# Kernel tuning notes

Hardware: AMD Instinct MI355X
Metric: run time of the kernel (lower is better)

The kernel has to match this reference:

```python
import jax, jax.numpy as jnp
import numpy as np

B, S, IN_DIM, OUT_DIM = 4, 4096, 512, 64


def setup_inputs() -> dict:
    key = jax.random.key(0)
    ks = jax.random.split(key, 8)
    scale = 1.0 / np.sqrt(IN_DIM)
    return {
        "input_embedding": jax.random.normal(ks[0], (B, S, IN_DIM), dtype=jnp.float32),
        "mask": jax.random.randint(ks[1], (S, S), 0, 2, dtype=jnp.int32),
        "Wq": jax.random.uniform(ks[2], (IN_DIM, OUT_DIM), jnp.float32, -scale, scale),
        "bq": jax.random.uniform(ks[3], (OUT_DIM,), jnp.float32, -scale, scale),
        "Wk": jax.random.uniform(ks[4], (IN_DIM, OUT_DIM), jnp.float32, -scale, scale),
        "bk": jax.random.uniform(ks[5], (OUT_DIM,), jnp.float32, -scale, scale),
        "Wv": jax.random.uniform(ks[6], (IN_DIM, OUT_DIM), jnp.float32, -scale, scale),
        "bv": jax.random.uniform(ks[7], (OUT_DIM,), jnp.float32, -scale, scale),
    }


def reference(input_embedding, mask, Wq, bq, Wk, bk, Wv, bv):
    # q,k,v: [B,S,D]
    q = jnp.einsum("bsi,id->bsd", input_embedding, Wq) + bq
    k = jnp.einsum("bsi,id->bsd", input_embedding, Wk) + bk
    v = jnp.einsum("bsi,id->bsd", input_embedding, Wv) + bv
    d_k = q.shape[-1]
    # scores: [B,S,S]
    scores = jnp.einsum("bqd,bkd->bqk", q, k) / jnp.sqrt(jnp.float32(d_k))
    # NOTE: original uses masked_fill(mask==0, 1e-6) on the SCORES (not -inf)
    scores = jnp.where(mask == 0, jnp.float32(1e-6), scores)
    probs = jax.nn.softmax(scores, axis=-1)
    return jnp.einsum("bqk,bkd->bqd", probs, v)
```

## Files before the change

### kernel.cpp

```cpp
#include <hip/hip_runtime.h>

#define BATCH 4
#define SEQ 4096
#define IND 512
#define DH 64
#define NSPLIT 8
#define QKVB 1024
#define MASKB 1366

typedef __attribute__((ext_vector_type(8))) _Float16 f16x8;
typedef __attribute__((ext_vector_type(4))) _Float16 f16x4;
typedef __attribute__((ext_vector_type(4))) float f32x4;
typedef unsigned long long u64;
typedef unsigned int u32;

#define MFMA16(a, b, c) __builtin_amdgcn_mfma_f32_16x16x32_f16(a, b, c, 0, 0, 0)
#define GLL16(g, l)                                                                  \
    __builtin_amdgcn_global_load_lds(                                                \
        (const __attribute__((address_space(1))) void*)(g),                          \
        (__attribute__((address_space(3))) void*)(l), 16, 0, 0)

__global__ __launch_bounds__(256) void wprep_kernel(
    const float* __restrict__ Wq, const float* __restrict__ bq,
    const float* __restrict__ Wk, const float* __restrict__ bk,
    const float* __restrict__ Wv, const float* __restrict__ bv,
    _Float16* __restrict__ Wt, float* __restrict__ bcat) {
    __shared__ float tile[64][65];
    const int bid = blockIdx.x, tid = threadIdx.x;
    const int mat = bid >> 3, k0 = (bid & 7) * 64;
    const float QS = 0.125f * 1.44269504088896f;
    const float* W = (mat == 0) ? Wq : ((mat == 1) ? Wk : Wv);
    const float scale = (mat == 0) ? QS : 1.0f;
    if (bid == 0 && tid < 192) {
        int m2 = tid >> 6, n = tid & 63;
        const float* bb = (m2 == 0) ? bq : ((m2 == 1) ? bk : bv);
        bcat[tid] = bb[n] * ((m2 == 0) ? QS : 1.0f);
    }
    const int n = tid & 63, r0 = tid >> 6;
#pragma unroll
    for (int i = 0; i < 16; ++i) {
        int r = r0 * 16 + i;
        tile[r][n] = W[(size_t)(k0 + r) * 64 + n];
    }
    __syncthreads();
    const int k = tid & 63, n0 = tid >> 6;
#pragma unroll
    for (int i = 0; i < 16; ++i) {
        int nn = n0 * 16 + i;
        Wt[(size_t)(mat * 64 + nn) * IND + k0 + k] = (_Float16)(tile[k][nn] * scale);
    }
}

__global__ __launch_bounds__(192) void qkv_mask_kernel(const float* __restrict__ X,
    const _Float16* __restrict__ Wt, const float* __restrict__ bcat,
    _Float16* __restrict__ Qh, _Float16* __restrict__ Kh, _Float16* __restrict__ Vt,
    const int* __restrict__ mask, u64* __restrict__ bits3) {
    __shared__ __align__(16) _Float16 xs[16 * 520];
    const int tid = threadIdx.x;
    const int w = tid >> 6, lane = tid & 63, l15 = lane & 15, g = lane >> 4;

    if (blockIdx.x >= QKVB) {
        int wv = (blockIdx.x - QKVB) * 3 + w;
        if (wv < 4096) {
            int kw = wv & 63, q0 = (wv >> 6) * 64;
            u64 keep = 0;
#pragma unroll 8
            for (int i = 0; i < 64; ++i) {
                int val = mask[(size_t)(q0 + i) * SEQ + kw * 64 + lane];
                u64 b = __ballot(val != 0);
                if (lane == i) keep = b;
            }
            bits3[((size_t)kw << 12) + q0 + lane] = keep;
        }
        return;
    }

    const int m0 = blockIdx.x * 16;
    const float4* src = (const float4*)(X + (size_t)m0 * IND);
#pragma unroll
    for (int u = 0; u < 11; ++u) {
        int idx = u * 192 + tid;
        if (idx < 2048) {
            float4 x = src[idx];
            int row = idx >> 7, c4 = idx & 127;
            f16x4 h;
            h[0] = (_Float16)x.x; h[1] = (_Float16)x.y;
            h[2] = (_Float16)x.z; h[3] = (_Float16)x.w;
            *(f16x4*)&xs[row * 520 + c4 * 4] = h;
        }
    }
    __syncthreads();

    f32x4 acc[4];
#pragma unroll
    for (int nt = 0; nt < 4; ++nt) acc[nt] = (f32x4){0.f, 0.f, 0.f, 0.f};

    const _Float16* Wm = Wt + (size_t)(w * 64 + l15) * IND + g * 8;
#pragma unroll
    for (int kc = 0; kc < 16; ++kc) {
        f16x8 a = *(const f16x8*)&xs[l15 * 520 + kc * 32 + g * 8];
#pragma unroll
        for (int nt = 0; nt < 4; ++nt)
            acc[nt] = MFMA16(a, *(const f16x8*)(Wm + kc * 32 + (size_t)nt * 16 * IND), acc[nt]);
    }

    const int b = m0 >> 12;
    const int sbase = (m0 & (SEQ - 1)) & ~31;
    const int hi = (m0 >> 4) & 1;
#pragma unroll
    for (int nt = 0; nt < 4; ++nt) {
        float bias = bcat[w * 64 + nt * 16 + l15];
        int ncol = nt * 16 + l15;
        if (w == 0) {
#pragma unroll
            for (int r = 0; r < 4; ++r)
                Qh[(size_t)(m0 + g * 4 + r) * DH + ncol] = (_Float16)(acc[nt][r] + bias);
        } else if (w == 1) {
#pragma unroll
            for (int r = 0; r < 4; ++r)
                Kh[(size_t)(m0 + g * 4 + r) * DH + ncol] = (_Float16)(acc[nt][r] + bias);
        } else {
            f16x4 vv;
#pragma unroll
            for (int r = 0; r < 4; ++r) vv[r] = (_Float16)(acc[nt][r] + bias);
            *(f16x4*)(Vt + ((size_t)b * DH + ncol) * SEQ + sbase + 8 * g + 4 * hi) = vv;
        }
    }
}

__global__ __launch_bounds__(256, 2) void flash_kernel(
    const _Float16* __restrict__ Qh, const _Float16* __restrict__ Kh,
    const _Float16* __restrict__ Vt, const u64* __restrict__ bits3,
    float* __restrict__ accP, float* __restrict__ lP) {
    constexpr int KPWT = SEQ / NSPLIT;
    constexpr int NT = KPWT / 64;
    __shared__ __align__(16) _Float16 ks[2][64 * 64];
    __shared__ __align__(16) _Float16 vs[2][64 * 64];

    const int tid = threadIdx.x;
    const int w = tid >> 6, lane = tid & 63, l15 = lane & 15, g = lane >> 4;
    const int bid = blockIdx.x;
    const int xcd = bid & 7, i = bid >> 3;
    const int b = xcd >> 1;
    const int split = (xcd & 1) * 4 + (i & 3);
    const int qblk = i >> 2;
    const int q0 = qblk * 256 + w * 64;
    const int k0base = split * KPWT;

    const _Float16* Qb = Qh + (size_t)b * SEQ * DH;
    const _Float16* Kb = Kh + (size_t)b * SEQ * DH;
    const _Float16* Vb = Vt + (size_t)b * DH * SEQ;
    const u64* bitsQ = bits3 + q0;

    const int tau = w * 1024 + lane * 16;
    const size_t vg0 = (size_t)(tau >> 7) * (SEQ * 2) + (tau & 127);
    _Float16* kl0 = &ks[0][w * 512];
    _Float16* kl1 = &ks[1][w * 512];
    _Float16* vl0 = &vs[0][w * 512];
    _Float16* vl1 = &vs[1][w * 512];

    f16x8 Qa[4][2];
#pragma unroll
    for (int mi = 0; mi < 4; ++mi)
#pragma unroll
        for (int kc = 0; kc < 2; ++kc)
            Qa[mi][kc] = *(const f16x8*)(Qb + (size_t)(q0 + mi * 16 + l15) * DH + kc * 32 + g * 8);

    f32x4 O[4][4];
    float lsum[4];
#pragma unroll
    for (int mi = 0; mi < 4; ++mi)
#pragma unroll
        for (int nd = 0; nd < 4; ++nd) O[mi][nd] = (f32x4){0.f, 0.f, 0.f, 0.f};
#pragma unroll
    for (int j = 0; j < 4; ++j) lsum[j] = 0.f;

    {
        const char* kg = (const char*)Kb + (size_t)k0base * 128 + tau;
        const char* vg = (const char*)Vb + vg0 + (size_t)k0base * 2;
        GLL16(kg, kl0);
        GLL16(kg + 4096, kl0 + 2048);
        GLL16(vg, vl0);
        GLL16(vg + (size_t)32 * SEQ * 2, vl0 + 2048);
    }
    __syncthreads();

#pragma unroll 2
    for (int t = 0; t < NT; ++t) {
        const int cur = t & 1;
        const int k0 = k0base + t * 64;
        const int kw = k0 >> 6;
        if (t + 1 < NT) {
            const char* kg = (const char*)Kb + (size_t)(k0 + 64) * 128 + tau;
            const char* vg = (const char*)Vb + vg0 + (size_t)(k0 + 64) * 2;
            _Float16* kl = cur ? kl0 : kl1;
            _Float16* vl = cur ? vl0 : vl1;
            GLL16(kg, kl);
            GLL16(kg + 4096, kl + 2048);
            GLL16(vg, vl);
            GLL16(vg + (size_t)32 * SEQ * 2, vl + 2048);
        }

        f16x8 Kf[4][2], Vf[4][2];
#pragma unroll
        for (int kk = 0; kk < 4; ++kk)
#pragma unroll
            for (int kc = 0; kc < 2; ++kc)
                Kf[kk][kc] = *(const f16x8*)&ks[cur][(kk * 16 + l15) * 64 + kc * 32 + g * 8];
#pragma unroll
        for (int nd = 0; nd < 4; ++nd)
#pragma unroll
            for (int h = 0; h < 2; ++h)
                Vf[nd][h] = *(const f16x8*)&vs[cur][(nd * 16 + l15) * 64 + h * 32 + g * 8];

#pragma unroll
        for (int mi = 0; mi < 4; ++mi) {
            u64 bw = bitsQ[((size_t)kw << 12) + mi * 16 + l15];
            f32x4 c0 = {0.f, 0.f, 0.f, 0.f}, c1 = {0.f, 0.f, 0.f, 0.f};
            f32x4 c2 = {0.f, 0.f, 0.f, 0.f}, c3 = {0.f, 0.f, 0.f, 0.f};
            c0 = MFMA16(Kf[0][0], Qa[mi][0], c0);
            c0 = MFMA16(Kf[0][1], Qa[mi][1], c0);
            c1 = MFMA16(Kf[1][0], Qa[mi][0], c1);
            c1 = MFMA16(Kf[1][1], Qa[mi][1], c1);
            c2 = MFMA16(Kf[2][0], Qa[mi][0], c2);
            c2 = MFMA16(Kf[2][1], Qa[mi][1], c2);
            c3 = MFMA16(Kf[3][0], Qa[mi][0], c3);
            c3 = MFMA16(Kf[3][1], Qa[mi][1], c3);
            u32 ms0 = (u32)(bw >> (4 * g));
            u32 ms1 = (u32)(bw >> (16 + 4 * g));
            u32 ms2 = (u32)(bw >> (32 + 4 * g));
            u32 ms3 = (u32)(bw >> (48 + 4 * g));
            f16x8 Pa0, Pa1;
            float ls = 0.f;
#pragma unroll
            for (int r = 0; r < 4; ++r) {
                float s0 = ((ms0 >> r) & 1u) ? c0[r] : 0.0f;
                float s1 = ((ms1 >> r) & 1u) ? c1[r] : 0.0f;
                float s2 = ((ms2 >> r) & 1u) ? c2[r] : 0.0f;
                float s3 = ((ms3 >> r) & 1u) ? c3[r] : 0.0f;
                float p0 = __builtin_amdgcn_exp2f(s0);
                float p1 = __builtin_amdgcn_exp2f(s1);
                float p2 = __builtin_amdgcn_exp2f(s2);
                float p3 = __builtin_amdgcn_exp2f(s3);
                ls += (p0 + p1) + (p2 + p3);
                Pa0[r] = (_Float16)p0;
                Pa0[r + 4] = (_Float16)p1;
                Pa1[r] = (_Float16)p2;
                Pa1[r + 4] = (_Float16)p3;
            }
            lsum[mi] += ls;
#pragma unroll
            for (int nd = 0; nd < 4; ++nd) {
                O[mi][nd] = MFMA16(Pa0, Vf[nd][0], O[mi][nd]);
                O[mi][nd] = MFMA16(Pa1, Vf[nd][1], O[mi][nd]);
            }
        }
        __syncthreads();
    }

#pragma unroll
    for (int j = 0; j < 4; ++j) {
        float v = lsum[j];
        v += __shfl_xor(v, 16);
        v += __shfl_xor(v, 32);
        lsum[j] = v;
    }
    float* accB = accP + ((size_t)split * BATCH + b) * SEQ * DH;
    float* lB = lP + ((size_t)split * BATCH + b) * SEQ;
    if (lane < 16) {
#pragma unroll
        for (int mi = 0; mi < 4; ++mi)
            lB[q0 + mi * 16 + l15] = lsum[mi];
    }
#pragma unroll
    for (int mi = 0; mi < 4; ++mi)
#pragma unroll
        for (int nd = 0; nd < 4; ++nd)
#pragma unroll
            for (int r = 0; r < 4; ++r)
                accB[(size_t)(q0 + mi * 16 + 4 * g + r) * DH + nd * 16 + l15] = O[mi][nd][r];
}

__global__ __launch_bounds__(256) void reduce_kernel(const float* __restrict__ accP,
                                                     const float* __restrict__ lP,
                                                     float* __restrict__ out) {
    int idx = blockIdx.x * 256 + threadIdx.x;
    int bq = idx >> 6, d = idx & 63;
    float a = 0.f, l = 0.f;
#pragma unroll
    for (int s = 0; s < NSPLIT; ++s) {
        a += accP[((size_t)s * BATCH * SEQ + bq) * DH + d];
        l += lP[(size_t)s * BATCH * SEQ + bq];
    }
    out[idx] = a / l;
}

extern "C" void kernel_launch(void* const* d_in, const int* in_sizes, int n_in,
                              void* d_out, int out_size, void* d_ws, size_t ws_size,
                              hipStream_t stream) {
    const float* X = (const float*)d_in[0];
    const int* mask = (const int*)d_in[1];
    const float* Wq = (const float*)d_in[2];
    const float* bq = (const float*)d_in[3];
    const float* Wk = (const float*)d_in[4];
    const float* bk = (const float*)d_in[5];
    const float* Wv = (const float*)d_in[6];
    const float* bv = (const float*)d_in[7];
    float* out = (float*)d_out;

    char* ws = (char*)d_ws;
    _Float16* Qh = (_Float16*)ws;
    _Float16* Kh = (_Float16*)(ws + (2u << 20));
    _Float16* Vt = (_Float16*)(ws + (4u << 20));
    u64* bits3 = (u64*)(ws + (6u << 20));
    float* accP = (float*)(ws + (8u << 20));
    float* lP = (float*)(ws + (40u << 20));
    _Float16* Wt = (_Float16*)(ws + (41u << 20));
    float* bcat = (float*)(ws + (41u << 20) + (256u << 10));

    wprep_kernel<<<dim3(24), dim3(256), 0, stream>>>(Wq, bq, Wk, bk, Wv, bv, Wt, bcat);
    qkv_mask_kernel<<<dim3(QKVB + MASKB), dim3(192), 0, stream>>>(X, Wt, bcat, Qh, Kh, Vt,
                                                                  mask, bits3);
    flash_kernel<<<dim3(512), dim3(256), 0, stream>>>(Qh, Kh, Vt, bits3, accP, lP);
    reduce_kernel<<<dim3(BATCH * SEQ * DH / 256), dim3(256), 0, stream>>>(accP, lP, out);
}
```

Before: 85.25 us.

## Double QKV projection rows per block, batch mask loads, schedule mask blocks first

The QKV projection blocks now handle 32 rows instead of 16. Each weight fragment loaded from global memory feeds two MFMAs, which halves weight traffic per row and halves the projection block count. The mask-packing path issues all 64 row loads up front before the ballots, exposing more memory-level parallelism at the cost of more registers. Mask blocks are placed first in the grid so the memory-bound mask work starts early and overlaps the projection blocks.

Result: no change. 86.03 us (+0.9%).

```diff
diff --git a/kernel.cpp b/kernel.cpp
--- a/kernel.cpp
+++ b/kernel.cpp
@@ -5,8 +5,8 @@
 #define IND 512
 #define DH 64
 #define NSPLIT 8
-#define QKVB 1024
 #define MASKB 1366
+#define QKVB 512
 
 typedef __attribute__((ext_vector_type(8))) _Float16 f16x8;
 typedef __attribute__((ext_vector_type(4))) _Float16 f16x4;
@@ -55,32 +55,35 @@
     const _Float16* __restrict__ Wt, const float* __restrict__ bcat,
     _Float16* __restrict__ Qh, _Float16* __restrict__ Kh, _Float16* __restrict__ Vt,
     const int* __restrict__ mask, u64* __restrict__ bits3) {
-    __shared__ __align__(16) _Float16 xs[16 * 520];
+    __shared__ __align__(16) _Float16 xs[32 * 520];
     const int tid = threadIdx.x;
     const int w = tid >> 6, lane = tid & 63, l15 = lane & 15, g = lane >> 4;
 
-    if (blockIdx.x >= QKVB) {
-        int wv = (blockIdx.x - QKVB) * 3 + w;
+    if (blockIdx.x < MASKB) {
+        int wv = blockIdx.x * 3 + w;
         if (wv < 4096) {
             int kw = wv & 63, q0 = (wv >> 6) * 64;
+            const int* mp = mask + (size_t)q0 * SEQ + kw * 64 + lane;
+            int v[64];
+#pragma unroll
+            for (int i = 0; i < 64; ++i) v[i] = mp[(size_t)i * SEQ];
             u64 keep = 0;
-#pragma unroll 8
+#pragma unroll
             for (int i = 0; i < 64; ++i) {
-                int val = mask[(size_t)(q0 + i) * SEQ + kw * 64 + lane];
-                u64 b = __ballot(val != 0);
-                if (lane == i) keep = b;
+                u64 b = __ballot(v[i] != 0);
+                keep = (lane == i) ? b : keep;
             }
             bits3[((size_t)kw << 12) + q0 + lane] = keep;
         }
         return;
     }
 
-    const int m0 = blockIdx.x * 16;
+    const int m0 = (blockIdx.x - MASKB) * 32;
     const float4* src = (const float4*)(X + (size_t)m0 * IND);
 #pragma unroll
-    for (int u = 0; u < 11; ++u) {
+    for (int u = 0; u < 22; ++u) {
         int idx = u * 192 + tid;
-        if (idx < 2048) {
+        if (idx < 4096) {
             float4 x = src[idx];
             int row = idx >> 7, c4 = idx & 127;
             f16x4 h;
@@ -91,39 +94,54 @@
     }
     __syncthreads();
 
-    f32x4 acc[4];
-#pragma unroll
-    for (int nt = 0; nt < 4; ++nt) acc[nt] = (f32x4){0.f, 0.f, 0.f, 0.f};
+    f32x4 acc0[4], acc1[4];
+#pragma unroll
+    for (int nt = 0; nt < 4; ++nt) {
+        acc0[nt] = (f32x4){0.f, 0.f, 0.f, 0.f};
+        acc1[nt] = (f32x4){0.f, 0.f, 0.f, 0.f};
+    }
 
     const _Float16* Wm = Wt + (size_t)(w * 64 + l15) * IND + g * 8;
 #pragma unroll
     for (int kc = 0; kc < 16; ++kc) {
-        f16x8 a = *(const f16x8*)&xs[l15 * 520 + kc * 32 + g * 8];
-#pragma unroll
-        for (int nt = 0; nt < 4; ++nt)
-            acc[nt] = MFMA16(a, *(const f16x8*)(Wm + kc * 32 + (size_t)nt * 16 * IND), acc[nt]);
+        f16x8 a0 = *(const f16x8*)&xs[l15 * 520 + kc * 32 + g * 8];
+        f16x8 a1 = *(const f16x8*)&xs[(16 + l15) * 520 + kc * 32 + g * 8];
+#pragma unroll
+        for (int nt = 0; nt < 4; ++nt) {
+            f16x8 wf = *(const f16x8*)(Wm + kc * 32 + (size_t)nt * 16 * IND);
+            acc0[nt] = MFMA16(a0, wf, acc0[nt]);
+            acc1[nt] = MFMA16(a1, wf, acc1[nt]);
+        }
     }
 
     const int b = m0 >> 12;
-    const int sbase = (m0 & (SEQ - 1)) & ~31;
-    const int hi = (m0 >> 4) & 1;
+    const int sbase = m0 & (SEQ - 1);
 #pragma unroll
     for (int nt = 0; nt < 4; ++nt) {
         float bias = bcat[w * 64 + nt * 16 + l15];
         int ncol = nt * 16 + l15;
         if (w == 0) {
 #pragma unroll
-            for (int r = 0; r < 4; ++r)
-                Qh[(size_t)(m0 + g * 4 + r) * DH + ncol] = (_Float16)(acc[nt][r] + bias);
+            for (int r = 0; r < 4; ++r) {
+                Qh[(size_t)(m0 + g * 4 + r) * DH + ncol] = (_Float16)(acc0[nt][r] + bias);
+                Qh[(size_t)(m0 + 16 + g * 4 + r) * DH + ncol] = (_Float16)(acc1[nt][r] + bias);
+            }
         } else if (w == 1) {
 #pragma unroll
-            for (int r = 0; r < 4; ++r)
-                Kh[(size_t)(m0 + g * 4 + r) * DH + ncol] = (_Float16)(acc[nt][r] + bias);
+            for (int r = 0; r < 4; ++r) {
+                Kh[(size_t)(m0 + g * 4 + r) * DH + ncol] = (_Float16)(acc0[nt][r] + bias);
+                Kh[(size_t)(m0 + 16 + g * 4 + r) * DH + ncol] = (_Float16)(acc1[nt][r] + bias);
+            }
         } else {
-            f16x4 vv;
-#pragma unroll
-            for (int r = 0; r < 4; ++r) vv[r] = (_Float16)(acc[nt][r] + bias);
-            *(f16x4*)(Vt + ((size_t)b * DH + ncol) * SEQ + sbase + 8 * g + 4 * hi) = vv;
+            f16x4 v0, v1;
+#pragma unroll
+            for (int r = 0; r < 4; ++r) {
+                v0[r] = (_Float16)(acc0[nt][r] + bias);
+                v1[r] = (_Float16)(acc1[nt][r] + bias);
+            }
+            _Float16* vb = Vt + ((size_t)b * DH + ncol) * SEQ + sbase + 8 * g;
+            *(f16x4*)(vb) = v0;
+            *(f16x4*)(vb + 4) = v1;
         }
     }
 }
@@ -319,7 +337,7 @@
     float* bcat = (float*)(ws + (41u << 20) + (256u << 10));
 
     wprep_kernel<<<dim3(24), dim3(256), 0, stream>>>(Wq, bq, Wk, bk, Wv, bv, Wt, bcat);
-    qkv_mask_kernel<<<dim3(QKVB + MASKB), dim3(192), 0, stream>>>(X, Wt, bcat, Qh, Kh, Vt,
+    qkv_mask_kernel<<<dim3(MASKB + QKVB), dim3(192), 0, stream>>>(X, Wt, bcat, Qh, Kh, Vt,
                                                                   mask, bits3);
     flash_kernel<<<dim3(512), dim3(256), 0, stream>>>(Qh, Kh, Vt, bits3, accP, lP);
     reduce_kernel<<<dim3(BATCH * SEQ * DH / 256), dim3(256), 0, stream>>>(accP, lP, out);
```
